# Performance work log

Measured on AMD Instinct MI355X. Metric: run time of the kernel, lower is better.

## Reference

```python
import jax, jax.numpy as jnp
import numpy as np
import math

RES = 1024          # FastTrigLookup / FastPhaseProcessor resolution
TWO_PI = 2.0 * math.pi
D = 512             # model dim


def setup_inputs() -> dict:
    key = jax.random.key(0)
    ks = jax.random.split(key, 4)
    B, L = 4, 4096

    def xavier(k, shape):
        fan_out, fan_in = shape
        std = math.sqrt(2.0 / (fan_in + fan_out))
        return jax.random.normal(k, shape, jnp.float32) * std

    return {
        "x": jax.random.normal(ks[0], (B, L, D), jnp.float32),
        "ft_w": xavier(ks[1], (2 * D, D)),
        "ft_b": jnp.zeros((2 * D,), jnp.float32),
        "ln_g": jnp.ones((2 * D,), jnp.float32),
        "ln_b": jnp.zeros((2 * D,), jnp.float32),
        "exc": jnp.ones((1,), jnp.float32) * 0.1,  # excitation_factor init
        "qkv_w": xavier(ks[2], (6 * D, 6 * D)),
        "qkv_b": jnp.zeros((6 * D,), jnp.float32),
        "op_w": xavier(ks[3], (2 * D, 2 * D)),
        "op_b": jnp.zeros((2 * D,), jnp.float32),
    }


def _forward(x, ft_w, ft_b, ln_g, ln_b, exc, qkv_w, qkv_b, op_w, op_b):
    B, L = x.shape[:2]
    sin_tab = jnp.sin(jnp.linspace(0.0, TWO_PI, RES)).astype(x.dtype)
    cos_tab = jnp.cos(jnp.linspace(0.0, TWO_PI, RES)).astype(x.dtype)

    # --- SimpleQuantumState: fused Linear -> tanh-GELU -> LayerNorm ---
    t = x @ ft_w.T + ft_b                                  # [B,L,2D]
    c1, c2 = 0.044715, math.sqrt(2.0 / math.pi)
    g = 0.5 * t * (1.0 + jnp.tanh(c2 * (t + c1 * t ** 3)))
    mu = g.mean(-1, keepdims=True)
    var = ((g - mu) ** 2).mean(-1, keepdims=True)
    n = (g - mu) * jax.lax.rsqrt(var + 1e-5) * ln_g + ln_b
    rp, ip = n[..., :D], n[..., D:]
    # atan2 -> gather-based sin/cos lookup (torch .long() truncates toward 0;
    # negative indices wrap from the end -> emulate with mod RES)
    ang = jnp.arctan2(ip + 1e-8, rp + 1e-8)
    idx = jnp.mod((ang / TWO_PI * (RES - 1)).astype(jnp.int32), RES)
    real = rp * cos_tab[idx]
    imag = ip * sin_tab[idx]
    nrm = jax.lax.rsqrt(real ** 2 + imag ** 2 + 1e-8) * math.sqrt(1.0 / D)
    real, imag = real * nrm, imag * nrm

    # --- EnhancedDynamicPhaseSpace: collapse prevention via trig lookup ---
    amp = jnp.sqrt(real ** 2 + imag ** 2 + 1e-8)
    coll = (amp < 0.1).astype(x.dtype)
    el = jnp.linspace(0.0, 1.0, D) * TWO_PI                # energy_levels * 2pi
    lidx = jnp.clip((jnp.mod(el, TWO_PI) / TWO_PI * RES).astype(jnp.int32), 0, RES - 1)
    real = real + coll * cos_tab[lidx] * exc
    imag = imag + coll * sin_tab[lidx] * exc
    nrm2 = jax.lax.rsqrt(real ** 2 + imag ** 2 + 1e-8)
    real, imag = real * nrm2, imag * nrm2

    # --- BasicQuantumAttention with q=k=v = quantum state (pad_mask=None) ---
    qkv_in = jnp.concatenate([real, imag, real, imag, real, imag], axis=-1)  # [B,L,6D]
    qkv = (qkv_in @ qkv_w.T + qkv_b).reshape(B, L, 6, D)
    q_r, k_r = qkv[:, :, 0], qkv[:, :, 2]
    v_r, v_i = qkv[:, :, 4], qkv[:, :, 5]
    scores = jnp.einsum('bld,bmd->blm', q_r, k_r) * (D ** -0.5)
    attn = jax.nn.softmax(scores, axis=-1)                 # dropout=eval -> identity
    o = jnp.concatenate([jnp.einsum('blm,bmd->bld', attn, v_r),
                         jnp.einsum('blm,bmd->bld', attn, v_i)], axis=-1)
    out = o @ op_w.T + op_b                                # [B,L,2D]
    return out


def reference(x, ft_w, ft_b, ln_g, ln_b, exc, qkv_w, qkv_b, op_w, op_b):
    out = _forward(x, ft_w, ft_b, ln_g, ln_b, exc, qkv_w, qkv_b, op_w, op_b)
    return (out[..., :D], out[..., D:])
```

## Files before the change

kernel.cpp:

```cpp
#include <hip/hip_runtime.h>
#include <hip/hip_bf16.h>
#include <math.h>


#define TWO_PI_F 6.283185307179586f

typedef __attribute__((ext_vector_type(4))) float f32x4;
typedef __attribute__((ext_vector_type(8))) short bf16x8;
typedef __attribute__((ext_vector_type(4))) unsigned short u16x4;
typedef __hip_bfloat16 bf16;

__device__ __forceinline__ void gl_lds16(const void* g, void* l) {
  __builtin_amdgcn_global_load_lds((const __attribute__((address_space(1))) void*)g,
                                   (__attribute__((address_space(3))) void*)l, 16, 0, 0);
}
__device__ __forceinline__ unsigned short f2bf_bits(float f) {
  union { __hip_bfloat16 h; unsigned short u; } cv;
  cv.h = __float2bfloat16(f);
  return cv.u;
}
__device__ __forceinline__ float bf_bits2f(unsigned short b) {
  union { unsigned int u; float f; } cv;
  cv.u = ((unsigned int)b) << 16;
  return cv.f;
}

template <int EPI, int ORD>
__global__ __launch_bounds__(256, 2) void gemm128(
    const bf16* __restrict__ A, const bf16* __restrict__ B, void* __restrict__ C,
    void* __restrict__ Cx, const float* __restrict__ bias, int K, int lda, int ldb, int ldc,
    float scale, long long zsa, long long zsb, long long zsc, float* __restrict__ P0,
    float* __restrict__ P1) {
  __shared__ __align__(16) bf16 smem[2 * 128 * 64];
  bf16* sA = smem;
  bf16* sB = smem + 128 * 64;
  const int tid = threadIdx.x;
  const int lane = tid & 63, wid = tid >> 6;
  const int wm = wid >> 1, wn = wid & 1;

  const int gx = gridDim.x, gy = gridDim.y;
  int flat = blockIdx.x + gx * (blockIdx.y + gy * blockIdx.z);
  {
    const int nwg = gx * gy * gridDim.z;
    const int q = nwg >> 3, r = nwg & 7;
    const int x = flat & 7, loc = flat >> 3;
    flat = (x < r ? x * (q + 1) : r * (q + 1) + (x - r) * q) + loc;
  }
  const int bx = flat % gx;
  const int by = (flat / gx) % gy;
  const int bz = flat / (gx * gy);
  const int bm = by * 128, bn = bx * 128;

  const bf16 *Az, *Bz;
  if constexpr (EPI == 5) {
    const int b = bz & 1, c = bz >> 1;
    Az = A + (long long)b * zsa + c * 2048;
    Bz = B + (long long)b * zsb + c * 2048;
  } else {
    Az = A + (long long)bz * zsa;
    Bz = B + (long long)bz * zsb;
  }

  f32x4 acc[4][4];
#pragma unroll
  for (int i = 0; i < 4; ++i)
#pragma unroll
    for (int j = 0; j < 4; ++j) acc[i][j] = (f32x4){0.f, 0.f, 0.f, 0.f};

  long long rowA[4], rowB[4];
#pragma unroll
  for (int t = 0; t < 4; ++t) {
    const int c = tid + 256 * t;
    const int r = c >> 3, s = c & 7;
    const int ga = ((s ^ (r & 7)) << 3);
    rowA[t] = (long long)(bm + r) * lda + ga;
    rowB[t] = (long long)(bn + r) * ldb + ga;
  }

  const int fr = lane & 15, ksl = lane >> 4;

  for (int k0 = 0; k0 < K; k0 += 64) {
#pragma unroll
    for (int t = 0; t < 4; ++t) gl_lds16(Az + rowA[t] + k0, &sA[(tid + 256 * t) * 8]);
#pragma unroll
    for (int t = 0; t < 4; ++t) gl_lds16(Bz + rowB[t] + k0, &sB[(tid + 256 * t) * 8]);
    __syncthreads();
    bf16x8 af[4][2], bfv[4][2];
#pragma unroll
    for (int i = 0; i < 4; ++i) {
      const int R = wm * 64 + i * 16 + fr;
#pragma unroll
      for (int kk = 0; kk < 2; ++kk) {
        const int s = (kk * 4 + ksl) ^ (R & 7);
        af[i][kk] = *(const bf16x8*)&sA[R * 64 + s * 8];
      }
    }
#pragma unroll
    for (int j = 0; j < 4; ++j) {
      const int R = wn * 64 + j * 16 + fr;
#pragma unroll
      for (int kk = 0; kk < 2; ++kk) {
        const int s = (kk * 4 + ksl) ^ (R & 7);
        bfv[j][kk] = *(const bf16x8*)&sB[R * 64 + s * 8];
      }
    }
#pragma unroll
    for (int kk = 0; kk < 2; ++kk)
#pragma unroll
      for (int i = 0; i < 4; ++i)
#pragma unroll
        for (int j = 0; j < 4; ++j) {
          if constexpr (ORD == 0)
            acc[i][j] =
                __builtin_amdgcn_mfma_f32_16x16x32_bf16(af[i][kk], bfv[j][kk], acc[i][j], 0, 0, 0);
          else
            acc[i][j] =
                __builtin_amdgcn_mfma_f32_16x16x32_bf16(bfv[j][kk], af[i][kk], acc[i][j], 0, 0, 0);
        }
    __syncthreads();
  }

  if constexpr (EPI == 4) {
    bf16* st = smem;
#pragma unroll
    for (int i = 0; i < 4; ++i)
#pragma unroll
      for (int j = 0; j < 4; ++j) {
        const int m0 = wm * 64 + i * 16 + ksl * 4;
        const int dl = wn * 64 + j * 16 + fr;
        const float bv = bias[bn + dl];
        u16x4 w;
#pragma unroll
        for (int r = 0; r < 4; ++r) w[r] = f2bf_bits(acc[i][j][r] * scale + bv);
        const int s = (m0 >> 2) ^ ((dl & 7) << 1);
        *(u16x4*)&st[dl * 128 + s * 4] = w;
      }
    __syncthreads();
    const int b = bm >> 12;
    const int mmb = bm & 4095;
#pragma unroll
    for (int tt = 0; tt < 8; ++tt) {
      const int idx = tt * 256 + tid;
      const int dl = idx >> 4;
      const int q = idx & 15;
      const int s = (2 * q) ^ ((dl & 7) << 1);
      const bf16x8 vv = *(const bf16x8*)&st[dl * 128 + s * 4];
      *(bf16x8*)((unsigned short*)Cx +
                 ((long long)(b * 1024 + bn + dl)) * 4096 + mmb + q * 8) = vv;
    }
  } else {
#pragma unroll
    for (int i = 0; i < 4; ++i)
#pragma unroll
      for (int j = 0; j < 4; ++j) {
        const int row = bm + wm * 64 + i * 16 + fr;
        const int col0 = bn + wn * 64 + j * 16 + ksl * 4;
        f32x4 v = acc[i][j];
#pragma unroll
        for (int r = 0; r < 4; ++r) v[r] *= scale;
        if constexpr (EPI == 0 || EPI == 1) {
          if (bias) {
            const f32x4 bv = *(const f32x4*)&bias[col0];
            v += bv;
          }
        }
        if constexpr (EPI == 1) {
#pragma unroll
          for (int r = 0; r < 4; ++r) {
            const float t = v[r];
            float y = 0.7978845608028654f * (t + 0.044715f * t * t * t);
            y = fminf(fmaxf(y, -15.f), 15.f);
            const float e = __expf(2.f * y);
            v[r] = t * e / (1.f + e);
          }
        }
        if constexpr (EPI == 3) {
          const f32x4 bv = *(const f32x4*)&bias[col0];
          v += bv;
          float* dst = (col0 < 512) ? (float*)C : (float*)Cx;
          const long long rout = (long long)bz * 4096 + row;
          *(f32x4*)&dst[rout * 512 + (col0 & 511)] = v;
        } else if constexpr (EPI == 5) {
          const int b = bz & 1, c = bz >> 1;
          if (c == 0) {
            const f32x4 bv = *(const f32x4*)&bias[col0];
            v += bv;
            float* dst = (col0 < 512) ? (float*)C : (float*)Cx;
            const long long rout = zsc + (long long)b * 4096 + row;
            *(f32x4*)&dst[rout * 512 + (col0 & 511)] = v;
          } else {
            float* dst = b ? P1 : P0;
            *(f32x4*)&dst[(long long)row * 1024 + col0] = v;
          }
        } else if constexpr (EPI == 2) {
          bf16* cc = (bf16*)C + (long long)bz * zsc;
          u16x4 w;
#pragma unroll
          for (int r = 0; r < 4; ++r) w[r] = f2bf_bits(v[r]);
          *(u16x4*)&cc[(long long)row * ldc + col0] = w;
        } else {
          bf16* cc = (bf16*)C;
          u16x4 w;
#pragma unroll
          for (int r = 0; r < 4; ++r) w[r] = f2bf_bits(v[r]);
          *(u16x4*)&cc[(long long)row * ldc + col0] = w;
        }
      }
  }
  (void)ldc;
}

__global__ __launch_bounds__(256) void combine_kernel(const float* __restrict__ p0,
                                                      const float* __restrict__ p1,
                                                      float* __restrict__ out0,
                                                      float* __restrict__ out1) {
  const int idx = blockIdx.x * 256 + threadIdx.x;
  const int b = idx >> 20;
  const int rem = idx & 1048575;
  const int row = rem >> 8;
  const int c4 = rem & 255;
  const float* p = b ? p1 : p0;
  const f32x4 v = *(const f32x4*)(p + (long long)row * 1024 + c4 * 4);
  float* dst = (c4 < 128) ? out0 : out1;
  const long long o = ((long long)(b * 4096 + row)) * 512 + (c4 & 127) * 4;
  f32x4 d = *(f32x4*)(dst + o);
  d += v;
  *(f32x4*)(dst + o) = d;
}

__global__ __launch_bounds__(256) void ln_phase_kernel(
    const bf16* __restrict__ g, bf16* __restrict__ u, const float* __restrict__ ln_g,
    const float* __restrict__ ln_b, const float* __restrict__ lcos,
    const float* __restrict__ lsin, const float* __restrict__ cost,
    const float* __restrict__ sint) {
  __shared__ float sg[1024];
  __shared__ float red[4];
  const int tid = threadIdx.x;
  const int lane = tid & 63, wid = tid >> 6;
  const long long row = blockIdx.x;
  const bf16* gr = g + row * 1024;

  const u16x4 raw = *(const u16x4*)(gr + tid * 4);
  float lv[4];
  float lsum = 0.f;
#pragma unroll
  for (int e = 0; e < 4; ++e) {
    lv[e] = bf_bits2f(raw[e]);
    lsum += lv[e];
  }
  *(f32x4*)&sg[tid * 4] = *(f32x4*)lv;
#pragma unroll
  for (int off = 32; off > 0; off >>= 1) lsum += __shfl_xor(lsum, off);
  if (lane == 0) red[wid] = lsum;
  __syncthreads();
  const float mu = (red[0] + red[1] + red[2] + red[3]) * (1.0f / 1024.0f);
  __syncthreads();
  float lvar = 0.f;
#pragma unroll
  for (int e = 0; e < 4; ++e) {
    const float d = lv[e] - mu;
    lvar += d * d;
  }
#pragma unroll
  for (int off = 32; off > 0; off >>= 1) lvar += __shfl_xor(lvar, off);
  if (lane == 0) red[wid] = lvar;
  __syncthreads();
  const float var = (red[0] + red[1] + red[2] + red[3]) * (1.0f / 1024.0f);
  const float rs = rsqrtf(var + 1e-5f);

#pragma unroll
  for (int kk = 0; kk < 2; ++kk) {
    const int p = tid + kk * 256;
    const float rp = (sg[p] - mu) * rs * ln_g[p] + ln_b[p];
    const float ip = (sg[p + 512] - mu) * rs * ln_g[p + 512] + ln_b[p + 512];
    const float ang = atan2f(ip + 1e-8f, rp + 1e-8f);
    int idx = (int)((ang / TWO_PI_F) * 1023.0f);
    idx = idx < 0 ? idx + 1024 : idx;
    float real = rp * cost[idx];
    float imag = ip * sint[idx];
    const float nrm = rsqrtf(real * real + imag * imag + 1e-8f) * 0.044194173824159216f;
    real *= nrm;
    imag *= nrm;
    const float amp = sqrtf(real * real + imag * imag + 1e-8f);
    const float coll = (amp < 0.1f) ? 1.0f : 0.0f;
    real += coll * lcos[p];
    imag += coll * lsin[p];
    const float n2 = rsqrtf(real * real + imag * imag + 1e-8f);
    u[row * 1024 + p] = __float2bfloat16(real * n2);
    u[row * 1024 + 512 + p] = __float2bfloat16(imag * n2);
  }
}

__global__ __launch_bounds__(256) void softmax_kernel(bf16* __restrict__ s) {
  __shared__ float red[4];
  const int tid = threadIdx.x;
  const int lane = tid & 63, wid = tid >> 6;
  bf16* sr = s + (long long)blockIdx.x * 4096;
  f32x4 f[4];
  float mx = -3.0e38f;
#pragma unroll
  for (int k = 0; k < 4; ++k) {
    const u16x4 raw = *(const u16x4*)(sr + (k * 256 + tid) * 4);
#pragma unroll
    for (int e = 0; e < 4; ++e) {
      f[k][e] = bf_bits2f(raw[e]);
      mx = fmaxf(mx, f[k][e]);
    }
  }
#pragma unroll
  for (int off = 32; off > 0; off >>= 1) mx = fmaxf(mx, __shfl_xor(mx, off));
  if (lane == 0) red[wid] = mx;
  __syncthreads();
  mx = fmaxf(fmaxf(red[0], red[1]), fmaxf(red[2], red[3]));
  __syncthreads();
  float sum = 0.f;
#pragma unroll
  for (int k = 0; k < 4; ++k)
#pragma unroll
    for (int e = 0; e < 4; ++e) {
      f[k][e] = __expf(f[k][e] - mx);
      sum += f[k][e];
    }
#pragma unroll
  for (int off = 32; off > 0; off >>= 1) sum += __shfl_xor(sum, off);
  if (lane == 0) red[wid] = sum;
  __syncthreads();
  const float inv = 1.0f / (red[0] + red[1] + red[2] + red[3]);
#pragma unroll
  for (int k = 0; k < 4; ++k) {
    u16x4 w;
#pragma unroll
    for (int e = 0; e < 4; ++e) w[e] = f2bf_bits(f[k][e] * inv);
    *(u16x4*)(sr + (k * 256 + tid) * 4) = w;
  }
}

__global__ __launch_bounds__(256) void fold_all(
    const float* __restrict__ w, const float* __restrict__ b,
    const float* __restrict__ op_w, const float* __restrict__ exc,
    const float* __restrict__ ft_w, const float* __restrict__ x, bf16* __restrict__ weff,
    bf16* __restrict__ wvT, float* __restrict__ beff, float* __restrict__ cost,
    float* __restrict__ sint, float* __restrict__ lcos, float* __restrict__ lsin,
    bf16* __restrict__ ftw_b, bf16* __restrict__ opw_b, bf16* __restrict__ x_b) {
  __shared__ float tile[32][33];
  __shared__ float red[4];
  const int blk = blockIdx.x;
  const int tid = threadIdx.x;
  if (blk < 4096) {
    const int i = blk * 256 + tid;
    const int o = i >> 10, j = i & 1023;
    const int so = (o < 512) ? o : o + 512;
    const float* wr = w + (long long)so * 3072;
    weff[i] = __float2bfloat16(wr[j] + wr[1024 + j] + wr[2048 + j]);
    if (j == 0) beff[o] = b[so];
  } else if (blk < 5120) {
    const int tb = blk - 4096;
    const int t0 = (tb & 31) * 32, j0 = (tb >> 5) * 32;
    const int tx = tid & 31, ty = tid >> 5;
#pragma unroll
    for (int k = 0; k < 4; ++k) {
      const int t = t0 + ty + k * 8;
      const float* wr = w + (long long)(2048 + t) * 3072 + j0 + tx;
      tile[ty + k * 8][tx] = wr[0] + wr[1024] + wr[2048];
    }
    __syncthreads();
#pragma unroll
    for (int k = 0; k < 4; ++k) {
      const int r = ty + k * 8;
      wvT[(long long)(j0 + r) * 1024 + t0 + tx] = __float2bfloat16(tile[tx][r]);
    }
  } else if (blk < 6144) {
    const int o = blk - 5120;
    const int lane = tid & 63, wid = tid >> 6;
    float s = 0.f;
#pragma unroll
    for (int k = 0; k < 4; ++k) {
      const int t = tid + k * 256;
      s += op_w[(long long)o * 1024 + t] * b[2048 + t];
    }
#pragma unroll
    for (int off = 32; off > 0; off >>= 1) s += __shfl_xor(s, off);
    if (lane == 0) red[wid] = s;
    __syncthreads();
    if (tid == 0) beff[1024 + o] = red[0] + red[1] + red[2] + red[3];
  } else if (blk == 6144) {
    const double step = 6.283185307179586 / 1023.0;
#pragma unroll
    for (int k = 0; k < 4; ++k) {
      const int i = tid + k * 256;
      const float a = (float)((double)i * step);
      cost[i] = cosf(a);
      sint[i] = sinf(a);
    }
#pragma unroll
    for (int k = 0; k < 2; ++k) {
      const int i = tid + k * 256;
      const float el = ((float)i / 511.0f) * TWO_PI_F;
      const float m = fmodf(el, TWO_PI_F);
      int li = (int)((m / TWO_PI_F) * 1024.0f);
      li = min(max(li, 0), 1023);
      const float a = (float)((double)li * step);
      lcos[i] = cosf(a) * exc[0];
      lsin[i] = sinf(a) * exc[0];
    }
  } else if (blk < 6657) {
    const long long q = (long long)(blk - 6145) * 256 + tid;
    const f32x4 f = *(const f32x4*)(ft_w + q * 4);
    u16x4 wv;
#pragma unroll
    for (int e = 0; e < 4; ++e) wv[e] = f2bf_bits(f[e]);
    *(u16x4*)((unsigned short*)ftw_b + q * 4) = wv;
  } else if (blk < 7681) {
    const long long q = (long long)(blk - 6657) * 256 + tid;
    const f32x4 f = *(const f32x4*)(op_w + q * 4);
    u16x4 wv;
#pragma unroll
    for (int e = 0; e < 4; ++e) wv[e] = f2bf_bits(f[e]);
    *(u16x4*)((unsigned short*)opw_b + q * 4) = wv;
  } else {
    const long long q0 = (long long)(blk - 7681) * 256 + tid;
#pragma unroll
    for (int t = 0; t < 4; ++t) {
      const long long q = q0 + (long long)t * 524288;
      const f32x4 f = *(const f32x4*)(x + q * 4);
      u16x4 wv;
#pragma unroll
      for (int e = 0; e < 4; ++e) wv[e] = f2bf_bits(f[e]);
      *(u16x4*)((unsigned short*)x_b + q * 4) = wv;
    }
  }
}

extern "C" void kernel_launch(void* const* d_in, const int* in_sizes, int n_in, void* d_out,
                              int out_size, void* d_ws, size_t ws_size, hipStream_t stream) {
  const float* x = (const float*)d_in[0];
  const float* ft_w = (const float*)d_in[1];
  const float* ft_b = (const float*)d_in[2];
  const float* ln_g = (const float*)d_in[3];
  const float* ln_b = (const float*)d_in[4];
  const float* exc = (const float*)d_in[5];
  const float* qkv_w = (const float*)d_in[6];
  const float* qkv_b = (const float*)d_in[7];
  const float* op_w = (const float*)d_in[8];
  const float* op_b = (const float*)d_in[9];

  char* ws = (char*)d_ws;
  const size_t MB = 1024ull * 1024ull;
  bf16* ftw_b = (bf16*)(ws + 0);
  bf16* weff = (bf16*)(ws + 1 * MB);
  bf16* opw_b = (bf16*)(ws + 5 * MB);
  bf16* wvT = (bf16*)(ws + 7 * MB);
  float* beff = (float*)(ws + 9 * MB);
  float* cost = (float*)(ws + 9 * MB + 8192);
  float* sint = (float*)(ws + 9 * MB + 12288);
  float* lcos = (float*)(ws + 9 * MB + 16384);
  float* lsin = (float*)(ws + 9 * MB + 18432);
  bf16* v2T = (bf16*)(ws + 10 * MB);
  bf16* qk = (bf16*)(ws + 42 * MB);
  bf16* x_b = (bf16*)(ws + 74 * MB);
  bf16* gbuf = (bf16*)(ws + 90 * MB);
  bf16* ubuf = (bf16*)(ws + 122 * MB);
  bf16* sc = (bf16*)(ws + 74 * MB);
  float* part0 = (float*)(ws + 138 * MB);
  float* part1 = (float*)(ws + 154 * MB);

  const bool big = ws_size >= 204 * MB;

  fold_all<<<9729, 256, 0, stream>>>(qkv_w, qkv_b, op_w, exc, ft_w, x, weff, wvT, beff, cost,
                                     sint, lcos, lsin, ftw_b, opw_b, x_b);

  gemm128<0, 1><<<dim3(8, 8), 256, 0, stream>>>(opw_b, wvT, weff + 1024 * 1024, nullptr,
                                                nullptr, 1024, 1024, 1024, 1024, 1.0f, 0, 0,
                                                0, nullptr, nullptr);
  gemm128<1, 1><<<dim3(8, 128), 256, 0, stream>>>(x_b, ftw_b, gbuf, nullptr, ft_b, 512, 512,
                                                  512, 1024, 1.0f, 0, 0, 0, nullptr, nullptr);
  ln_phase_kernel<<<16384, 256, 0, stream>>>(gbuf, ubuf, ln_g, ln_b, lcos, lsin, cost, sint);
  gemm128<0, 1><<<dim3(8, 128), 256, 0, stream>>>(ubuf, weff, qk, nullptr, beff, 1024, 1024,
                                                  1024, 1024, 1.0f, 0, 0, 0, nullptr, nullptr);
  gemm128<4, 0><<<dim3(8, 128), 256, 0, stream>>>(ubuf, weff + 1024 * 1024, nullptr, v2T,
                                                  beff + 1024, 1024, 1024, 1024, 0, 1.0f, 0,
                                                  0, 0, nullptr, nullptr);

  float* out0 = (float*)d_out;
  float* out1 = out0 + 8388608LL;
  if (big) {
    gemm128<2, 1><<<dim3(32, 32, 4), 256, 0, stream>>>(
        qk, qk + 512, sc, nullptr, nullptr, 512, 1024, 1024, 4096, 0.04419417382415922f,
        4096LL * 1024, 4096LL * 1024, 4096LL * 4096, nullptr, nullptr);
    softmax_kernel<<<16384, 256, 0, stream>>>(sc);
    gemm128<3, 1><<<dim3(8, 32, 4), 256, 0, stream>>>(
        sc, v2T, out0, out1, op_b, 4096, 4096, 4096, 0, 1.0f, 4096LL * 4096, 1024LL * 4096,
        0, nullptr, nullptr);
  } else {
    for (int p = 0; p < 2; ++p) {
      const bf16* qbase = qk + (long long)(2 * p) * 4096 * 1024;
      gemm128<2, 1><<<dim3(32, 32, 2), 256, 0, stream>>>(
          qbase, qbase + 512, sc, nullptr, nullptr, 512, 1024, 1024, 4096,
          0.04419417382415922f, 4096LL * 1024, 4096LL * 1024, 4096LL * 4096, nullptr,
          nullptr);
      softmax_kernel<<<8192, 256, 0, stream>>>(sc);
      gemm128<5, 1><<<dim3(8, 32, 4), 256, 0, stream>>>(
          sc, v2T + (long long)(2 * p) * 1024 * 4096, out0, out1, op_b, 2048, 4096, 4096, 0,
          1.0f, 4096LL * 4096, 1024LL * 4096, (long long)(2 * p) * 4096, part0, part1);
      combine_kernel<<<8192, 256, 0, stream>>>(part0, part1,
                                               out0 + (long long)(2 * p) * 4096 * 512,
                                               out1 + (long long)(2 * p) * 4096 * 512);
    }
  }
  (void)in_sizes;
  (void)n_in;
  (void)out_size;
}
```

Before: 428.5 us.

## Merge QK and V projection GEMMs into one launch; single-pass LayerNorm stats

Replaces the two separate GEMM launches that produce the QK projection and the transposed V projection with one launch of a new epilogue variant over a doubled N grid. Blocks pick the MFMA operand order and the epilogue (row-major with bias vs. transposed bf16 store) at runtime from their column index. The LayerNorm kernel now computes mean and mean-square in one reduction, which removes one barrier and one reduction pass. The runtime branch in the inner MFMA loop may cost code size or registers, and E[x^2]-mu^2 is less numerically stable than the two-pass variance.

```diff
diff --git a/kernel.cpp b/kernel.cpp
--- a/kernel.cpp
+++ b/kernel.cpp
@@ -61,6 +61,12 @@
     Bz = B + (long long)bz * zsb;
   }
 
+  bool useAB;
+  if constexpr (EPI == 6)
+    useAB = (bn >= 1024);
+  else
+    useAB = (ORD == 0);
+
   f32x4 acc[4][4];
 #pragma unroll
   for (int i = 0; i < 4; ++i)
@@ -104,23 +110,29 @@
         bfv[j][kk] = *(const bf16x8*)&sB[R * 64 + s * 8];
       }
     }
-#pragma unroll
-    for (int kk = 0; kk < 2; ++kk)
-#pragma unroll
-      for (int i = 0; i < 4; ++i)
-#pragma unroll
-        for (int j = 0; j < 4; ++j) {
-          if constexpr (ORD == 0)
+    if (useAB) {
+#pragma unroll
+      for (int kk = 0; kk < 2; ++kk)
+#pragma unroll
+        for (int i = 0; i < 4; ++i)
+#pragma unroll
+          for (int j = 0; j < 4; ++j)
             acc[i][j] =
                 __builtin_amdgcn_mfma_f32_16x16x32_bf16(af[i][kk], bfv[j][kk], acc[i][j], 0, 0, 0);
-          else
+    } else {
+#pragma unroll
+      for (int kk = 0; kk < 2; ++kk)
+#pragma unroll
+        for (int i = 0; i < 4; ++i)
+#pragma unroll
+          for (int j = 0; j < 4; ++j)
             acc[i][j] =
                 __builtin_amdgcn_mfma_f32_16x16x32_bf16(bfv[j][kk], af[i][kk], acc[i][j], 0, 0, 0);
-        }
+    }
     __syncthreads();
   }
 
-  if constexpr (EPI == 4) {
+  if ((EPI == 6) && useAB) {
     bf16* st = smem;
 #pragma unroll
     for (int i = 0; i < 4; ++i)
@@ -138,6 +150,7 @@
     __syncthreads();
     const int b = bm >> 12;
     const int mmb = bm & 4095;
+    const int d0 = bn - 1024;
 #pragma unroll
     for (int tt = 0; tt < 8; ++tt) {
       const int idx = tt * 256 + tid;
@@ -146,7 +159,7 @@
       const int s = (2 * q) ^ ((dl & 7) << 1);
       const bf16x8 vv = *(const bf16x8*)&st[dl * 128 + s * 4];
       *(bf16x8*)((unsigned short*)Cx +
-                 ((long long)(b * 1024 + bn + dl)) * 4096 + mmb + q * 8) = vv;
+                 ((long long)(b * 1024 + d0 + dl)) * 4096 + mmb + q * 8) = vv;
     }
   } else {
 #pragma unroll
@@ -158,7 +171,7 @@
         f32x4 v = acc[i][j];
 #pragma unroll
         for (int r = 0; r < 4; ++r) v[r] *= scale;
-        if constexpr (EPI == 0 || EPI == 1) {
+        if constexpr (EPI == 0 || EPI == 1 || EPI == 6) {
           if (bias) {
             const f32x4 bv = *(const f32x4*)&bias[col0];
             v += bv;
@@ -234,7 +247,7 @@
     const float* __restrict__ lsin, const float* __restrict__ cost,
     const float* __restrict__ sint) {
   __shared__ float sg[1024];
-  __shared__ float red[4];
+  __shared__ float red[4], red2[4];
   const int tid = threadIdx.x;
   const int lane = tid & 63, wid = tid >> 6;
   const long long row = blockIdx.x;
@@ -242,30 +255,27 @@
 
   const u16x4 raw = *(const u16x4*)(gr + tid * 4);
   float lv[4];
-  float lsum = 0.f;
+  float lsum = 0.f, lsq = 0.f;
 #pragma unroll
   for (int e = 0; e < 4; ++e) {
     lv[e] = bf_bits2f(raw[e]);
     lsum += lv[e];
+    lsq += lv[e] * lv[e];
   }
   *(f32x4*)&sg[tid * 4] = *(f32x4*)lv;
 #pragma unroll
-  for (int off = 32; off > 0; off >>= 1) lsum += __shfl_xor(lsum, off);
-  if (lane == 0) red[wid] = lsum;
+  for (int off = 32; off > 0; off >>= 1) {
+    lsum += __shfl_xor(lsum, off);
+    lsq += __shfl_xor(lsq, off);
+  }
+  if (lane == 0) {
+    red[wid] = lsum;
+    red2[wid] = lsq;
+  }
   __syncthreads();
   const float mu = (red[0] + red[1] + red[2] + red[3]) * (1.0f / 1024.0f);
-  __syncthreads();
-  float lvar = 0.f;
-#pragma unroll
-  for (int e = 0; e < 4; ++e) {
-    const float d = lv[e] - mu;
-    lvar += d * d;
-  }
-#pragma unroll
-  for (int off = 32; off > 0; off >>= 1) lvar += __shfl_xor(lvar, off);
-  if (lane == 0) red[wid] = lvar;
-  __syncthreads();
-  const float var = (red[0] + red[1] + red[2] + red[3]) * (1.0f / 1024.0f);
+  const float ex2 = (red2[0] + red2[1] + red2[2] + red2[3]) * (1.0f / 1024.0f);
+  const float var = ex2 - mu * mu;
   const float rs = rsqrtf(var + 1e-5f);
 
 #pragma unroll
@@ -475,11 +485,9 @@
   gemm128<1, 1><<<dim3(8, 128), 256, 0, stream>>>(x_b, ftw_b, gbuf, nullptr, ft_b, 512, 512,
                                                   512, 1024, 1.0f, 0, 0, 0, nullptr, nullptr);
   ln_phase_kernel<<<16384, 256, 0, stream>>>(gbuf, ubuf, ln_g, ln_b, lcos, lsin, cost, sint);
-  gemm128<0, 1><<<dim3(8, 128), 256, 0, stream>>>(ubuf, weff, qk, nullptr, beff, 1024, 1024,
-                                                  1024, 1024, 1.0f, 0, 0, 0, nullptr, nullptr);
-  gemm128<4, 0><<<dim3(8, 128), 256, 0, stream>>>(ubuf, weff + 1024 * 1024, nullptr, v2T,
-                                                  beff + 1024, 1024, 1024, 1024, 0, 1.0f, 0,
-                                                  0, 0, nullptr, nullptr);
+  gemm128<6, 1><<<dim3(16, 128), 256, 0, stream>>>(ubuf, weff, qk, v2T, beff, 1024, 1024,
+                                                   1024, 1024, 1.0f, 0, 0, 0, nullptr,
+                                                   nullptr);
 
   float* out0 = (float*)d_out;
   float* out1 = out0 + 8388608LL;
```

Result: slower. 463.2 us (+8.1%).
